# Performance work log

Hardware: AMD Instinct MI355X
Metric: run time of the kernel (lower is better)

## Reference

```python
import jax, jax.numpy as jnp
import numpy as np
from jax import lax

SAMPLE_RATE = 44100.0

def _shelf_coeffs(gain_db, fc, q, sr, high):
    # RBJ cookbook shelf biquad; high=True -> high_shelf, else low_shelf
    A = 10.0 ** (gain_db / 40.0)
    w0 = 2.0 * jnp.pi * (fc / sr)
    alpha = jnp.sin(w0) / (2.0 * q)
    c = jnp.cos(w0)
    sA = jnp.sqrt(A)
    sgn = 1.0 if high else -1.0
    b0 = A * (A + 1 + sgn * (A - 1) * c + 2 * sA * alpha)
    b1 = -2.0 * sgn * A * (A - 1 + sgn * (A + 1) * c)
    b2 = A * (A + 1 + sgn * (A - 1) * c - 2 * sA * alpha)
    a0 = A + 1 - sgn * (A - 1) * c + 2 * sA * alpha
    a1 = 2.0 * sgn * (A - 1 - sgn * (A + 1) * c)
    a2 = A + 1 - sgn * (A - 1) * c - 2 * sA * alpha
    b = jnp.stack([b0, b1, b2]) / a0
    a = jnp.stack([a0, a1, a2]) / a0
    return b, a

def _peaking_coeffs(gain_db, fc, q, sr):
    A = 10.0 ** (gain_db / 40.0)
    w0 = 2.0 * jnp.pi * (fc / sr)
    alpha = jnp.sin(w0) / (2.0 * q)
    c = jnp.cos(w0)
    b0 = 1 + alpha * A
    b1 = -2.0 * c
    b2 = 1 - alpha * A
    a0 = 1 + alpha / A
    a1 = -2.0 * c
    a2 = 1 - alpha / A
    b = jnp.stack([b0, b1, b2]) / a0
    a = jnp.stack([a0, a1, a2]) / a0
    return b, a

def _biquad_lfilter(b, a, x):
    # scipy.signal.lfilter with zero initial conditions, transposed DF-II.
    # x: (chs, T); state s: (chs, 2)
    b0, b1, b2 = b[0], b[1], b[2]
    a1, a2 = a[1], a[2]
    def step(s, xn):  # xn: (chs,)
        s1, s2 = s[:, 0], s[:, 1]
        yn = b0 * xn + s1
        s1n = b1 * xn - a1 * yn + s2
        s2n = b2 * xn - a2 * yn
        return jnp.stack([s1n, s2n], axis=1), yn
    s0 = jnp.zeros((x.shape[0], 2), x.dtype)
    _, y = lax.scan(step, s0, x.T)  # y: (T, chs)
    return y.T

def setup_inputs() -> dict:
    key = jax.random.key(0)
    x = jax.random.normal(key, (8, 2097152), dtype=jnp.float32)
    # rows: [low_shelf, band1, band2, band3, high_shelf]; cols: [gain_db, cutoff_hz, Q]
    eq_params = jnp.array([
        [3.0, 100.0, 0.9],
        [-2.5, 400.0, 1.2],
        [4.0, 1000.0, 2.0],
        [-5.0, 4000.0, 0.7],
        [2.5, 12000.0, 0.707],
    ], dtype=jnp.float32)
    return {"x": x, "eq_params": eq_params}

def reference(x, eq_params):
    sr = SAMPLE_RATE
    # low shelf
    b, a = _shelf_coeffs(eq_params[0, 0], eq_params[0, 1], eq_params[0, 2], sr, high=False)
    y = _biquad_lfilter(b, a, x)
    # 3 peaking bands
    for i in range(1, 4):
        b, a = _peaking_coeffs(eq_params[i, 0], eq_params[i, 1], eq_params[i, 2], sr)
        y = _biquad_lfilter(b, a, y)
    # high shelf
    b, a = _shelf_coeffs(eq_params[4, 0], eq_params[4, 1], eq_params[4, 2], sr, high=True)
    y = _biquad_lfilter(b, a, y)
    return y.astype(jnp.float32)
```

## Files before the change

kernel.cpp:

```cpp
#include <hip/hip_runtime.h>

#define SRATE 44100.0
#define WIN 16
#define NWIN 4
#define STRIDE 17
#define NBLK 1024
#define BLK_PER_CH 128

#ifndef M_PI
#define M_PI 3.14159265358979323846
#endif

struct CoefD { double b0, b1, b2, a1, a2; };

__device__ void cascade_step_d(const CoefD* cf, double* s, double x) {
    double u = x;
    #pragma unroll
    for (int i = 0; i < 5; i++) {
        double y   = cf[i].b0 * u + s[2*i];
        double s1n = cf[i].b1 * u - cf[i].a1 * y + s[2*i+1];
        double s2n = cf[i].b2 * u - cf[i].a2 * y;
        s[2*i]   = s1n;
        s[2*i+1] = s2n;
        u = y;
    }
}

__global__ __launch_bounds__(128) void k0_setup(const float* __restrict__ eqp,
                                                float* __restrict__ coef_f,
                                                float* __restrict__ mats_f) {
    __shared__ CoefD cf[5];
    __shared__ double M[100];
    int t = threadIdx.x;

    if (t == 0) {
        for (int i = 0; i < 5; i++) {
            double g  = (double)eqp[i*3 + 0];
            double fc = (double)eqp[i*3 + 1];
            double q  = (double)eqp[i*3 + 2];
            double A  = pow(10.0, g / 40.0);
            double w0 = 2.0 * M_PI * (fc / SRATE);
            double al = sin(w0) / (2.0 * q);
            double c  = cos(w0);
            double b0, b1, b2, a0, a1, a2;
            if (i == 0 || i == 4) {
                double sgn = (i == 4) ? 1.0 : -1.0;
                double sA = sqrt(A);
                b0 = A * ((A + 1.0) + sgn * (A - 1.0) * c + 2.0 * sA * al);
                b1 = -2.0 * sgn * A * ((A - 1.0) + sgn * (A + 1.0) * c);
                b2 = A * ((A + 1.0) + sgn * (A - 1.0) * c - 2.0 * sA * al);
                a0 = (A + 1.0) - sgn * (A - 1.0) * c + 2.0 * sA * al;
                a1 = 2.0 * sgn * ((A - 1.0) - sgn * (A + 1.0) * c);
                a2 = (A + 1.0) - sgn * (A - 1.0) * c - 2.0 * sA * al;
            } else {
                b0 = 1.0 + al * A; b1 = -2.0 * c; b2 = 1.0 - al * A;
                a0 = 1.0 + al / A; a1 = -2.0 * c; a2 = 1.0 - al / A;
            }
            cf[i].b0 = b0 / a0; cf[i].b1 = b1 / a0; cf[i].b2 = b2 / a0;
            cf[i].a1 = a1 / a0; cf[i].a2 = a2 / a0;
            coef_f[i*5 + 0] = (float)(b0 / a0);
            coef_f[i*5 + 1] = (float)(b1 / a0);
            coef_f[i*5 + 2] = (float)(b2 / a0);
            coef_f[i*5 + 3] = (float)(a1 / a0);
            coef_f[i*5 + 4] = (float)(a2 / a0);
        }
    }
    __syncthreads();

    if (t < 10) {
        double s[10];
        for (int k = 0; k < 10; k++) s[k] = (k == t) ? 1.0 : 0.0;
        cascade_step_d(cf, s, 0.0);
        for (int r = 0; r < 10; r++) M[r*10 + t] = s[r];
    }
    __syncthreads();

    for (int k = 1; k <= 20; k++) {
        double val = 0.0;
        if (t < 100) {
            int r = t / 10, c = t % 10;
            for (int j = 0; j < 10; j++) val += M[r*10 + j] * M[j*10 + c];
        }
        __syncthreads();
        if (t < 100) {
            M[t] = val;
            if (k >= 6 && k <= 13) mats_f[(k-6)*100 + t]         = (float)val;
            if (k >= 14)           mats_f[800 + (k-14)*100 + t]  = (float)val;
        }
        __syncthreads();
    }
}

__global__ __launch_bounds__(256, 4) void k1_fused(const float* __restrict__ x,
                                                   const float* __restrict__ coef,
                                                   const float* __restrict__ mats_f,
                                                   float* __restrict__ ibuf,
                                                   float* __restrict__ abuf) {
    __shared__ union SmemU {
        float stage[2][256 * STRIDE];
        struct { float M[800]; float buf[256][11]; } scan;
    } sm;
    int t = threadIdx.x, b = blockIdx.x;

    float cb0[5], cb1[5], cb2[5], ca1[5], ca2[5];
    #pragma unroll
    for (int i = 0; i < 5; i++) {
        cb0[i] = coef[i*5+0]; cb1[i] = coef[i*5+1]; cb2[i] = coef[i*5+2];
        ca1[i] = coef[i*5+3]; ca2[i] = coef[i*5+4];
    }
    const float4* x4 = (const float4*)x;
    const size_t base4 = (size_t)b * 4096;
    const int cb = t >> 2, q = t & 3;

    float4 rr[4];
    #pragma unroll
    for (int k = 0; k < 4; k++)
        rr[k] = x4[base4 + (size_t)(cb + 64*k) * 16 + q];
    #pragma unroll
    for (int k = 0; k < 4; k++) {
        int o = (cb + 64*k) * STRIDE + q*4;
        sm.stage[0][o+0] = rr[k].x; sm.stage[0][o+1] = rr[k].y;
        sm.stage[0][o+2] = rr[k].z; sm.stage[0][o+3] = rr[k].w;
    }
    __syncthreads();

    float s[10];
    #pragma unroll
    for (int k = 0; k < 10; k++) s[k] = 0.0f;

    for (int w = 0; w < NWIN; w++) {
        if (w + 1 < NWIN) {
            #pragma unroll
            for (int k = 0; k < 4; k++)
                rr[k] = x4[base4 + (size_t)(cb + 64*k) * 16 + (w+1)*4 + q];
        }
        const float* cur = sm.stage[w & 1] + t * STRIDE;
        #pragma unroll
        for (int i = 0; i < WIN; i++) {
            float u = cur[i];
            #pragma unroll
            for (int st = 0; st < 5; st++) {
                float y  = fmaf(cb0[st], u, s[2*st]);
                float t1 = fmaf(cb1[st], u, s[2*st+1]);
                s[2*st+1] = fmaf(-ca2[st], y, cb2[st] * u);
                s[2*st]   = fmaf(-ca1[st], y, t1);
                u = y;
            }
        }
        if (w + 1 < NWIN) {
            float* nb = sm.stage[(w+1) & 1];
            #pragma unroll
            for (int k = 0; k < 4; k++) {
                int o = (cb + 64*k) * STRIDE + q*4;
                nb[o+0] = rr[k].x; nb[o+1] = rr[k].y;
                nb[o+2] = rr[k].z; nb[o+3] = rr[k].w;
            }
        }
        __syncthreads();
    }

    for (int i = t; i < 800; i += 256) sm.scan.M[i] = mats_f[i];
    #pragma unroll
    for (int r = 0; r < 10; r++) sm.scan.buf[t][r] = s[r];
    __syncthreads();

    for (int d = 0; d < 8; d++) {
        float nv[10];
        bool act = (t >= (1 << d));
        if (act) {
            int src = t - (1 << d);
            #pragma unroll
            for (int r = 0; r < 10; r++) {
                float acc = s[r];
                #pragma unroll
                for (int k = 0; k < 10; k++)
                    acc = fmaf(sm.scan.M[d*100 + r*10 + k], sm.scan.buf[src][k], acc);
                nv[r] = acc;
            }
        }
        __syncthreads();
        if (act) {
            #pragma unroll
            for (int r = 0; r < 10; r++) { s[r] = nv[r]; sm.scan.buf[t][r] = nv[r]; }
        }
        __syncthreads();
    }

    #pragma unroll
    for (int r = 0; r < 10; r++)
        ibuf[(size_t)b * 2560 + r * 256 + t] = (t > 0) ? sm.scan.buf[t-1][r] : 0.0f;
    if (t == 255) {
        #pragma unroll
        for (int r = 0; r < 10; r++) abuf[b * 10 + r] = s[r];
    }
}

__global__ __launch_bounds__(128) void k2b_scan(const float* __restrict__ mats_f,
                                                const float* __restrict__ abuf,
                                                float* __restrict__ bbuf) {
    __shared__ float Qds[700];
    __shared__ float buf[128][11];
    int t = threadIdx.x, ch = blockIdx.x;
    int g = ch * 128 + t;

    for (int k = t; k < 700; k += 128) Qds[k] = mats_f[800 + k];

    float v[10];
    #pragma unroll
    for (int r = 0; r < 10; r++) { v[r] = abuf[g * 10 + r]; buf[t][r] = v[r]; }
    __syncthreads();

    for (int e = 0; e < 7; e++) {
        float nv[10];
        bool act = (t >= (1 << e));
        if (act) {
            int src = t - (1 << e);
            #pragma unroll
            for (int r = 0; r < 10; r++) {
                float acc = v[r];
                #pragma unroll
                for (int k = 0; k < 10; k++)
                    acc = fmaf(Qds[e*100 + r*10 + k], buf[src][k], acc);
                nv[r] = acc;
            }
        }
        __syncthreads();
        if (act) {
            #pragma unroll
            for (int r = 0; r < 10; r++) { v[r] = nv[r]; buf[t][r] = nv[r]; }
        }
        __syncthreads();
    }
    #pragma unroll
    for (int r = 0; r < 10; r++)
        bbuf[g * 10 + r] = (t > 0) ? buf[t-1][r] : 0.0f;
}

__global__ __launch_bounds__(256, 4) void k3_final(const float* __restrict__ x,
                                                   const float* __restrict__ coef,
                                                   const float* __restrict__ mats_f,
                                                   const float* __restrict__ ibuf,
                                                   const float* __restrict__ bbuf,
                                                   float* __restrict__ out) {
    __shared__ float inb[2][256 * STRIDE];
    __shared__ float Mds[800];
    int t = threadIdx.x, b = blockIdx.x;

    const float4* x4 = (const float4*)x;
    float4* o4 = (float4*)out;
    const size_t base4 = (size_t)b * 4096;
    const int cb = t >> 2, q = t & 3;

    float4 rr[4];
    #pragma unroll
    for (int k = 0; k < 4; k++)
        rr[k] = x4[base4 + (size_t)(cb + 64*k) * 16 + q];

    for (int i = t; i < 800; i += 256) Mds[i] = mats_f[i];

    float cb0[5], cb1[5], cb2[5], ca1[5], ca2[5];
    #pragma unroll
    for (int i = 0; i < 5; i++) {
        cb0[i] = coef[i*5+0]; cb1[i] = coef[i*5+1]; cb2[i] = coef[i*5+2];
        ca1[i] = coef[i*5+3]; ca2[i] = coef[i*5+4];
    }

    float s[10];
    #pragma unroll
    for (int r = 0; r < 10; r++)
        s[r] = ibuf[(size_t)b * 2560 + r * 256 + t];
    float v[10];
    #pragma unroll
    for (int r = 0; r < 10; r++) v[r] = bbuf[b * 10 + r];

    #pragma unroll
    for (int k = 0; k < 4; k++) {
        int o = (cb + 64*k) * STRIDE + q*4;
        inb[0][o+0] = rr[k].x; inb[0][o+1] = rr[k].y;
        inb[0][o+2] = rr[k].z; inb[0][o+3] = rr[k].w;
    }
    __syncthreads();

    for (int d = 0; d < 8; d++) {
        float wv[10];
        #pragma unroll
        for (int r = 0; r < 10; r++) {
            float acc = 0.0f;
            #pragma unroll
            for (int k = 0; k < 10; k++)
                acc = fmaf(Mds[d*100 + r*10 + k], v[k], acc);
            wv[r] = acc;
        }
        bool bit = (t >> d) & 1;
        #pragma unroll
        for (int r = 0; r < 10; r++) v[r] = bit ? wv[r] : v[r];
    }
    #pragma unroll
    for (int r = 0; r < 10; r++) s[r] += v[r];

    for (int w = 0; w < NWIN; w++) {
        if (w + 1 < NWIN) {
            #pragma unroll
            for (int k = 0; k < 4; k++)
                rr[k] = x4[base4 + (size_t)(cb + 64*k) * 16 + (w+1)*4 + q];
        }
        float* cur = inb[w & 1] + t * STRIDE;
        #pragma unroll
        for (int i = 0; i < WIN; i++) {
            float u = cur[i];
            #pragma unroll
            for (int st = 0; st < 5; st++) {
                float y  = fmaf(cb0[st], u, s[2*st]);
                float t1 = fmaf(cb1[st], u, s[2*st+1]);
                s[2*st+1] = fmaf(-ca2[st], y, cb2[st] * u);
                s[2*st]   = fmaf(-ca1[st], y, t1);
                u = y;
            }
            cur[i] = u;
        }
        if (w + 1 < NWIN) {
            float* nb = inb[(w+1) & 1];
            #pragma unroll
            for (int k = 0; k < 4; k++) {
                int o = (cb + 64*k) * STRIDE + q*4;
                nb[o+0] = rr[k].x; nb[o+1] = rr[k].y;
                nb[o+2] = rr[k].z; nb[o+3] = rr[k].w;
            }
        }
        __syncthreads();

        const float* sb = inb[w & 1];
        #pragma unroll
        for (int k = 0; k < 4; k++) {
            int o = (cb + 64*k) * STRIDE + q*4;
            float4 ov = make_float4(sb[o+0], sb[o+1], sb[o+2], sb[o+3]);
            o4[base4 + (size_t)(cb + 64*k) * 16 + (size_t)w*4 + q] = ov;
        }
    }
}

extern "C" void kernel_launch(void* const* d_in, const int* in_sizes, int n_in,
                              void* d_out, int out_size, void* d_ws, size_t ws_size,
                              hipStream_t stream) {
    const float* x   = (const float*)d_in[0];
    const float* eqp = (const float*)d_in[1];
    float* out = (float*)d_out;
    char* ws = (char*)d_ws;

    float* coef_f = (float*)ws;
    float* mats_f = (float*)(ws + 256);
    float* ibuf   = (float*)(ws + 8192);
    float* abuf   = (float*)(ws + 8192 + 10485760);
    float* bbuf   = (float*)(ws + 8192 + 10485760 + 40960);

    hipLaunchKernelGGL(k0_setup, dim3(1), dim3(128), 0, stream, eqp, coef_f, mats_f);
    hipLaunchKernelGGL(k1_fused, dim3(NBLK), dim3(256), 0, stream, x, coef_f, mats_f, ibuf, abuf);
    hipLaunchKernelGGL(k2b_scan, dim3(8), dim3(128), 0, stream, mats_f, abuf, bbuf);
    hipLaunchKernelGGL(k3_final, dim3(NBLK), dim3(256), 0, stream,
                       x, coef_f, mats_f, ibuf, bbuf, out);
}
```

Baseline: 174.3 us.

## Fuse block-level carry scan into final kernel and read scan matrices from global

Removes the separate 8-block k2b_scan launch. Each k3_final block now redundantly runs the 128-element per-channel carry scan over abuf in shared memory and takes its own prefix. Scan matrices are read directly from global/constant-like memory instead of being staged into LDS in k1 and k3, and k0 computes the five filter coefficient sets in parallel threads. This trades one launch and a global round trip for redundant scan work in every block and uncached-in-LDS matrix reads.

```diff
diff --git a/kernel.cpp b/kernel.cpp
--- a/kernel.cpp
+++ b/kernel.cpp
@@ -33,37 +33,36 @@
     __shared__ double M[100];
     int t = threadIdx.x;
 
-    if (t == 0) {
-        for (int i = 0; i < 5; i++) {
-            double g  = (double)eqp[i*3 + 0];
-            double fc = (double)eqp[i*3 + 1];
-            double q  = (double)eqp[i*3 + 2];
-            double A  = pow(10.0, g / 40.0);
-            double w0 = 2.0 * M_PI * (fc / SRATE);
-            double al = sin(w0) / (2.0 * q);
-            double c  = cos(w0);
-            double b0, b1, b2, a0, a1, a2;
-            if (i == 0 || i == 4) {
-                double sgn = (i == 4) ? 1.0 : -1.0;
-                double sA = sqrt(A);
-                b0 = A * ((A + 1.0) + sgn * (A - 1.0) * c + 2.0 * sA * al);
-                b1 = -2.0 * sgn * A * ((A - 1.0) + sgn * (A + 1.0) * c);
-                b2 = A * ((A + 1.0) + sgn * (A - 1.0) * c - 2.0 * sA * al);
-                a0 = (A + 1.0) - sgn * (A - 1.0) * c + 2.0 * sA * al;
-                a1 = 2.0 * sgn * ((A - 1.0) - sgn * (A + 1.0) * c);
-                a2 = (A + 1.0) - sgn * (A - 1.0) * c - 2.0 * sA * al;
-            } else {
-                b0 = 1.0 + al * A; b1 = -2.0 * c; b2 = 1.0 - al * A;
-                a0 = 1.0 + al / A; a1 = -2.0 * c; a2 = 1.0 - al / A;
-            }
-            cf[i].b0 = b0 / a0; cf[i].b1 = b1 / a0; cf[i].b2 = b2 / a0;
-            cf[i].a1 = a1 / a0; cf[i].a2 = a2 / a0;
-            coef_f[i*5 + 0] = (float)(b0 / a0);
-            coef_f[i*5 + 1] = (float)(b1 / a0);
-            coef_f[i*5 + 2] = (float)(b2 / a0);
-            coef_f[i*5 + 3] = (float)(a1 / a0);
-            coef_f[i*5 + 4] = (float)(a2 / a0);
-        }
+    if (t < 5) {
+        int i = t;
+        double g  = (double)eqp[i*3 + 0];
+        double fc = (double)eqp[i*3 + 1];
+        double q  = (double)eqp[i*3 + 2];
+        double A  = pow(10.0, g / 40.0);
+        double w0 = 2.0 * M_PI * (fc / SRATE);
+        double al = sin(w0) / (2.0 * q);
+        double c  = cos(w0);
+        double b0, b1, b2, a0, a1, a2;
+        if (i == 0 || i == 4) {
+            double sgn = (i == 4) ? 1.0 : -1.0;
+            double sA = sqrt(A);
+            b0 = A * ((A + 1.0) + sgn * (A - 1.0) * c + 2.0 * sA * al);
+            b1 = -2.0 * sgn * A * ((A - 1.0) + sgn * (A + 1.0) * c);
+            b2 = A * ((A + 1.0) + sgn * (A - 1.0) * c - 2.0 * sA * al);
+            a0 = (A + 1.0) - sgn * (A - 1.0) * c + 2.0 * sA * al;
+            a1 = 2.0 * sgn * ((A - 1.0) - sgn * (A + 1.0) * c);
+            a2 = (A + 1.0) - sgn * (A - 1.0) * c - 2.0 * sA * al;
+        } else {
+            b0 = 1.0 + al * A; b1 = -2.0 * c; b2 = 1.0 - al * A;
+            a0 = 1.0 + al / A; a1 = -2.0 * c; a2 = 1.0 - al / A;
+        }
+        cf[i].b0 = b0 / a0; cf[i].b1 = b1 / a0; cf[i].b2 = b2 / a0;
+        cf[i].a1 = a1 / a0; cf[i].a2 = a2 / a0;
+        coef_f[i*5 + 0] = (float)(b0 / a0);
+        coef_f[i*5 + 1] = (float)(b1 / a0);
+        coef_f[i*5 + 2] = (float)(b2 / a0);
+        coef_f[i*5 + 3] = (float)(a1 / a0);
+        coef_f[i*5 + 4] = (float)(a2 / a0);
     }
     __syncthreads();
 
@@ -98,7 +97,7 @@
                                                    float* __restrict__ abuf) {
     __shared__ union SmemU {
         float stage[2][256 * STRIDE];
-        struct { float M[800]; float buf[256][11]; } scan;
+        float buf[256][11];
     } sm;
     int t = threadIdx.x, b = blockIdx.x;
 
@@ -159,144 +158,145 @@
         __syncthreads();
     }
 
-    for (int i = t; i < 800; i += 256) sm.scan.M[i] = mats_f[i];
-    #pragma unroll
-    for (int r = 0; r < 10; r++) sm.scan.buf[t][r] = s[r];
+    #pragma unroll
+    for (int r = 0; r < 10; r++) sm.buf[t][r] = s[r];
     __syncthreads();
 
     for (int d = 0; d < 8; d++) {
+        const float* __restrict__ Mg = mats_f + d*100;
         float nv[10];
         bool act = (t >= (1 << d));
         if (act) {
             int src = t - (1 << d);
+            float bs[10];
+            #pragma unroll
+            for (int k = 0; k < 10; k++) bs[k] = sm.buf[src][k];
             #pragma unroll
             for (int r = 0; r < 10; r++) {
                 float acc = s[r];
                 #pragma unroll
                 for (int k = 0; k < 10; k++)
-                    acc = fmaf(sm.scan.M[d*100 + r*10 + k], sm.scan.buf[src][k], acc);
+                    acc = fmaf(Mg[r*10 + k], bs[k], acc);
                 nv[r] = acc;
             }
         }
         __syncthreads();
         if (act) {
             #pragma unroll
-            for (int r = 0; r < 10; r++) { s[r] = nv[r]; sm.scan.buf[t][r] = nv[r]; }
+            for (int r = 0; r < 10; r++) { s[r] = nv[r]; sm.buf[t][r] = nv[r]; }
         }
         __syncthreads();
     }
 
     #pragma unroll
     for (int r = 0; r < 10; r++)
-        ibuf[(size_t)b * 2560 + r * 256 + t] = (t > 0) ? sm.scan.buf[t-1][r] : 0.0f;
+        ibuf[(size_t)b * 2560 + r * 256 + t] = (t > 0) ? sm.buf[t-1][r] : 0.0f;
     if (t == 255) {
         #pragma unroll
         for (int r = 0; r < 10; r++) abuf[b * 10 + r] = s[r];
     }
 }
 
-__global__ __launch_bounds__(128) void k2b_scan(const float* __restrict__ mats_f,
-                                                const float* __restrict__ abuf,
-                                                float* __restrict__ bbuf) {
-    __shared__ float Qds[700];
-    __shared__ float buf[128][11];
-    int t = threadIdx.x, ch = blockIdx.x;
-    int g = ch * 128 + t;
-
-    for (int k = t; k < 700; k += 128) Qds[k] = mats_f[800 + k];
+__global__ __launch_bounds__(256, 4) void k3_final(const float* __restrict__ x,
+                                                   const float* __restrict__ coef,
+                                                   const float* __restrict__ mats_f,
+                                                   const float* __restrict__ ibuf,
+                                                   const float* __restrict__ abuf,
+                                                   float* __restrict__ out) {
+    __shared__ union SmemU {
+        float inb[2][256 * STRIDE];
+        struct { float pad[256 * STRIDE]; float sbuf[128][11]; } scn;
+    } sm;
+    int t = threadIdx.x, b = blockIdx.x;
+    const int ch = b >> 7;
+    const int ci = b & 127;
+
+    const float4* x4 = (const float4*)x;
+    float4* o4 = (float4*)out;
+    const size_t base4 = (size_t)b * 4096;
+    const int cb = t >> 2, q = t & 3;
+
+    float4 rr[4];
+    #pragma unroll
+    for (int k = 0; k < 4; k++)
+        rr[k] = x4[base4 + (size_t)(cb + 64*k) * 16 + q];
+
+    float cb0[5], cb1[5], cb2[5], ca1[5], ca2[5];
+    #pragma unroll
+    for (int i = 0; i < 5; i++) {
+        cb0[i] = coef[i*5+0]; cb1[i] = coef[i*5+1]; cb2[i] = coef[i*5+2];
+        ca1[i] = coef[i*5+3]; ca2[i] = coef[i*5+4];
+    }
+
+    float s[10];
+    #pragma unroll
+    for (int r = 0; r < 10; r++)
+        s[r] = ibuf[(size_t)b * 2560 + r * 256 + t];
+
+    #pragma unroll
+    for (int k = 0; k < 4; k++) {
+        int o = (cb + 64*k) * STRIDE + q*4;
+        sm.inb[0][o+0] = rr[k].x; sm.inb[0][o+1] = rr[k].y;
+        sm.inb[0][o+2] = rr[k].z; sm.inb[0][o+3] = rr[k].w;
+    }
+    for (int idx = t; idx < 1280; idx += 256)
+        sm.scn.sbuf[idx / 10][idx % 10] = abuf[(size_t)ch * 1280 + idx];
+    __syncthreads();
 
     float v[10];
-    #pragma unroll
-    for (int r = 0; r < 10; r++) { v[r] = abuf[g * 10 + r]; buf[t][r] = v[r]; }
-    __syncthreads();
-
+    if (t < 128) {
+        #pragma unroll
+        for (int r = 0; r < 10; r++) v[r] = sm.scn.sbuf[t][r];
+    }
     for (int e = 0; e < 7; e++) {
+        const float* __restrict__ Qg = mats_f + 800 + e*100;
         float nv[10];
-        bool act = (t >= (1 << e));
+        bool act = (t < 128) && (t >= (1 << e));
         if (act) {
             int src = t - (1 << e);
+            float bs[10];
+            #pragma unroll
+            for (int k = 0; k < 10; k++) bs[k] = sm.scn.sbuf[src][k];
             #pragma unroll
             for (int r = 0; r < 10; r++) {
                 float acc = v[r];
                 #pragma unroll
                 for (int k = 0; k < 10; k++)
-                    acc = fmaf(Qds[e*100 + r*10 + k], buf[src][k], acc);
+                    acc = fmaf(Qg[r*10 + k], bs[k], acc);
                 nv[r] = acc;
             }
         }
         __syncthreads();
         if (act) {
             #pragma unroll
-            for (int r = 0; r < 10; r++) { v[r] = nv[r]; buf[t][r] = nv[r]; }
-        }
-        __syncthreads();
-    }
+            for (int r = 0; r < 10; r++) { v[r] = nv[r]; sm.scn.sbuf[t][r] = nv[r]; }
+        }
+        __syncthreads();
+    }
+
+    float bp[10];
     #pragma unroll
     for (int r = 0; r < 10; r++)
-        bbuf[g * 10 + r] = (t > 0) ? buf[t-1][r] : 0.0f;
-}
-
-__global__ __launch_bounds__(256, 4) void k3_final(const float* __restrict__ x,
-                                                   const float* __restrict__ coef,
-                                                   const float* __restrict__ mats_f,
-                                                   const float* __restrict__ ibuf,
-                                                   const float* __restrict__ bbuf,
-                                                   float* __restrict__ out) {
-    __shared__ float inb[2][256 * STRIDE];
-    __shared__ float Mds[800];
-    int t = threadIdx.x, b = blockIdx.x;
-
-    const float4* x4 = (const float4*)x;
-    float4* o4 = (float4*)out;
-    const size_t base4 = (size_t)b * 4096;
-    const int cb = t >> 2, q = t & 3;
-
-    float4 rr[4];
-    #pragma unroll
-    for (int k = 0; k < 4; k++)
-        rr[k] = x4[base4 + (size_t)(cb + 64*k) * 16 + q];
-
-    for (int i = t; i < 800; i += 256) Mds[i] = mats_f[i];
-
-    float cb0[5], cb1[5], cb2[5], ca1[5], ca2[5];
-    #pragma unroll
-    for (int i = 0; i < 5; i++) {
-        cb0[i] = coef[i*5+0]; cb1[i] = coef[i*5+1]; cb2[i] = coef[i*5+2];
-        ca1[i] = coef[i*5+3]; ca2[i] = coef[i*5+4];
-    }
-
-    float s[10];
-    #pragma unroll
-    for (int r = 0; r < 10; r++)
-        s[r] = ibuf[(size_t)b * 2560 + r * 256 + t];
-    float v[10];
-    #pragma unroll
-    for (int r = 0; r < 10; r++) v[r] = bbuf[b * 10 + r];
-
-    #pragma unroll
-    for (int k = 0; k < 4; k++) {
-        int o = (cb + 64*k) * STRIDE + q*4;
-        inb[0][o+0] = rr[k].x; inb[0][o+1] = rr[k].y;
-        inb[0][o+2] = rr[k].z; inb[0][o+3] = rr[k].w;
-    }
+        bp[r] = (ci > 0) ? sm.scn.sbuf[ci-1][r] : 0.0f;
     __syncthreads();
 
     for (int d = 0; d < 8; d++) {
+        const float* __restrict__ Mg = mats_f + d*100;
         float wv[10];
         #pragma unroll
         for (int r = 0; r < 10; r++) {
             float acc = 0.0f;
             #pragma unroll
             for (int k = 0; k < 10; k++)
-                acc = fmaf(Mds[d*100 + r*10 + k], v[k], acc);
+                acc = fmaf(Mg[r*10 + k], bp[k], acc);
             wv[r] = acc;
         }
         bool bit = (t >> d) & 1;
         #pragma unroll
-        for (int r = 0; r < 10; r++) v[r] = bit ? wv[r] : v[r];
-    }
-    #pragma unroll
-    for (int r = 0; r < 10; r++) s[r] += v[r];
+        for (int r = 0; r < 10; r++) bp[r] = bit ? wv[r] : bp[r];
+    }
+    #pragma unroll
+    for (int r = 0; r < 10; r++) s[r] += bp[r];
 
     for (int w = 0; w < NWIN; w++) {
         if (w + 1 < NWIN) {
@@ -304,7 +304,7 @@
             for (int k = 0; k < 4; k++)
                 rr[k] = x4[base4 + (size_t)(cb + 64*k) * 16 + (w+1)*4 + q];
         }
-        float* cur = inb[w & 1] + t * STRIDE;
+        float* cur = sm.inb[w & 1] + t * STRIDE;
         #pragma unroll
         for (int i = 0; i < WIN; i++) {
             float u = cur[i];
@@ -319,7 +319,7 @@
             cur[i] = u;
         }
         if (w + 1 < NWIN) {
-            float* nb = inb[(w+1) & 1];
+            float* nb = sm.inb[(w+1) & 1];
             #pragma unroll
             for (int k = 0; k < 4; k++) {
                 int o = (cb + 64*k) * STRIDE + q*4;
@@ -329,7 +329,7 @@
         }
         __syncthreads();
 
-        const float* sb = inb[w & 1];
+        const float* sb = sm.inb[w & 1];
         #pragma unroll
         for (int k = 0; k < 4; k++) {
             int o = (cb + 64*k) * STRIDE + q*4;
@@ -351,11 +351,9 @@
     float* mats_f = (float*)(ws + 256);
     float* ibuf   = (float*)(ws + 8192);
     float* abuf   = (float*)(ws + 8192 + 10485760);
-    float* bbuf   = (float*)(ws + 8192 + 10485760 + 40960);
 
     hipLaunchKernelGGL(k0_setup, dim3(1), dim3(128), 0, stream, eqp, coef_f, mats_f);
     hipLaunchKernelGGL(k1_fused, dim3(NBLK), dim3(256), 0, stream, x, coef_f, mats_f, ibuf, abuf);
-    hipLaunchKernelGGL(k2b_scan, dim3(8), dim3(128), 0, stream, mats_f, abuf, bbuf);
     hipLaunchKernelGGL(k3_final, dim3(NBLK), dim3(256), 0, stream,
-                       x, coef_f, mats_f, ibuf, bbuf, out);
-}
+                       x, coef_f, mats_f, ibuf, abuf, out);
+}
```

Result: no change. 173.7 us (-0.3%).
